# Optimization experiments

Hardware: AMD Instinct MI355X
Metric: run time of the kernel (lower is better)

## Reference

```python
import jax, jax.numpy as jnp
import numpy as np

SIGMA = 1.0
TOP_K = 4

def setup_inputs() -> dict:
    key = jax.random.key(0)
    k1, k2, k3, k4 = jax.random.split(key, 4)
    B, N, IN_DIM, OUT_DIM, P = 2, 4096, 128, 128, 3
    x = jax.random.normal(k1, (B, N, IN_DIM), dtype=jnp.float32)
    pos = jax.random.normal(k2, (B, N, P), dtype=jnp.float32)
    # Linear(in_dim, out_dim): W [in_dim, out_dim], b [out_dim]
    lim = 1.0 / np.sqrt(IN_DIM)
    W = jax.random.uniform(k3, (IN_DIM, OUT_DIM), minval=-lim, maxval=lim, dtype=jnp.float32)
    b = jax.random.uniform(k4, (OUT_DIM,), minval=-lim, maxval=lim, dtype=jnp.float32)
    return {"x": x, "pos": pos, "W": W, "b": b}

def reference(x, pos, W, b):
    B, N, _ = x.shape
    # pairwise distances [B, N, N]
    pos_diff = pos[:, :, None, :] - pos[:, None, :, :]
    dist = jnp.sqrt(jnp.sum(pos_diff ** 2, axis=-1) + 1e-8)
    adj = jnp.exp(-dist ** 2 / (2.0 * SIGMA ** 2))
    # top-k mask along last dim
    _, indices = jax.lax.top_k(adj, TOP_K)  # [B, N, k]
    b_idx = jnp.arange(B)[:, None, None]
    n_idx = jnp.arange(N)[None, :, None]
    mask = jnp.zeros_like(adj).at[b_idx, n_idx, indices].set(1.0)
    adj = adj * mask
    adj = adj / (jnp.sum(adj, axis=-1, keepdims=True) + 1e-8)
    # weighted aggregation + linear
    out = jnp.einsum('bnm,bmd->bnd', adj, x)
    return out @ W + b
```

## Files before the change

### kernel.cpp

```cpp
#include <hip/hip_runtime.h>
#include <hip/hip_bf16.h>

#define NPTS 4096
#define NROWS 8192
#define DIM 128
#define CAP 8

typedef __attribute__((ext_vector_type(8))) short bf16x8;
typedef __attribute__((ext_vector_type(4))) float f32x4;

__global__ __launch_bounds__(256) void prep(const float* __restrict__ pos,
                                            const float* __restrict__ W,
                                            float4* __restrict__ pos4,
                                            __hip_bfloat16* __restrict__ Wt) {
    int t = blockIdx.x * 256 + threadIdx.x;
    if (t < NROWS) {
        const float* p = pos + (size_t)t * 3;
        pos4[t] = make_float4(p[0], p[1], p[2], 0.f);
    } else if (t < NROWS + DIM * DIM) {
        int i = t - NROWS;
        int n = i >> 7, k = i & 127;
        Wt[i] = __float2bfloat16(W[k * DIM + n]);
    }
}

__global__ __launch_bounds__(256) void xw_mfma(const float* __restrict__ x,
                                               const __hip_bfloat16* __restrict__ Wt,
                                               __hip_bfloat16* __restrict__ xWb) {
    int wave = threadIdx.x >> 6;
    int lane = threadIdx.x & 63;
    int tile = blockIdx.x * 4 + wave;
    int m0 = (tile >> 3) << 4;
    int n0 = (tile & 7) << 4;
    int r = lane & 15;
    int kg = lane >> 4;
    const float* xr = x + (size_t)(m0 + r) * DIM + kg * 8;
    const __hip_bfloat16* br = Wt + (size_t)(n0 + r) * DIM + kg * 8;
    f32x4 acc = {0.f, 0.f, 0.f, 0.f};
#pragma unroll
    for (int kb = 0; kb < 4; ++kb) {
        float4 a0 = *(const float4*)(xr + kb * 32);
        float4 a1 = *(const float4*)(xr + kb * 32 + 4);
        bf16x8 af;
        union { __hip_bfloat16 h; short s; } u;
        u.h = __float2bfloat16(a0.x); af[0] = u.s;
        u.h = __float2bfloat16(a0.y); af[1] = u.s;
        u.h = __float2bfloat16(a0.z); af[2] = u.s;
        u.h = __float2bfloat16(a0.w); af[3] = u.s;
        u.h = __float2bfloat16(a1.x); af[4] = u.s;
        u.h = __float2bfloat16(a1.y); af[5] = u.s;
        u.h = __float2bfloat16(a1.z); af[6] = u.s;
        u.h = __float2bfloat16(a1.w); af[7] = u.s;
        bf16x8 bfr = *(const bf16x8*)(br + kb * 32);
        acc = __builtin_amdgcn_mfma_f32_16x16x32_bf16(af, bfr, acc, 0, 0, 0);
    }
    int col = n0 + r;
    int rbase = m0 + (kg << 2);
#pragma unroll
    for (int reg = 0; reg < 4; ++reg)
        xWb[(size_t)(rbase + reg) * DIM + col] = __float2bfloat16(acc[reg]);
}

__device__ __forceinline__ float dist2(float4 q, float4 p) {
    float dx = q.x - p.x, dy = q.y - p.y, dz = q.z - p.z;
    return fmaf(dx, dx, fmaf(dy, dy, dz * dz));
}

__device__ __forceinline__ void vins(float& k0, float& k1, float& k2, float& k3,
                                     float s) {
    float c = fmaxf(k0, s); k0 = fminf(k0, s);
    float t = fmaxf(k1, c); k1 = fminf(k1, c); c = t;
    t = fmaxf(k2, c);       k2 = fminf(k2, c); c = t;
    k3 = fminf(k3, c);
}

__device__ __forceinline__ void vmerge(float& a0, float& a1, float& a2, float& a3,
                                       float b0, float b1, float b2, float b3) {
    float m0 = fminf(a0, b3), m1 = fminf(a1, b2);
    float m2 = fminf(a2, b1), m3 = fminf(a3, b0);
    float t0 = fminf(m0, m2), t2 = fmaxf(m0, m2);
    float t1 = fminf(m1, m3), t3 = fmaxf(m1, m3);
    a0 = fminf(t0, t1); a1 = fmaxf(t0, t1);
    a2 = fminf(t2, t3); a3 = fmaxf(t2, t3);
}

__global__ __launch_bounds__(256, 8) void topk_agg(const float4* __restrict__ pos4,
                                                   const __hip_bfloat16* __restrict__ xWb,
                                                   const float* __restrict__ bias,
                                                   float* __restrict__ out) {
    int lane = threadIdx.x & 63;
    int wave = threadIdx.x >> 6;
    int group = wave >> 1;
    int half = wave & 1;
    int rowbase = blockIdx.x * 4 + group * 2;
    int batch = rowbase >> 12;
    int ibase = rowbase & (NPTS - 1);
    const float4* pb = pos4 + (size_t)batch * NPTS;

    __shared__ float    vx[2][2][2][4];
    __shared__ unsigned hidx[2][2][2][CAP];
    __shared__ float    hdva[2][2][2][CAP];
    __shared__ unsigned hcnt[2][2][2];
    __shared__ unsigned fidx[2][2][4];
    __shared__ float    fdst[2][2][4];

    float4 q0 = pb[ibase], q1 = pb[ibase + 1];
    const float INF = __int_as_float(0x7f800000);
    float a0 = INF, a1 = INF, a2 = INF, a3 = INF;
    float b0 = INF, b1 = INF, b2 = INF, b3 = INF;
    int jbase = (half << 11) + lane;

#pragma unroll 4
    for (int t = 0; t < 32; ++t) {
        float4 p = pb[jbase + (t << 6)];
        vins(a0, a1, a2, a3, dist2(q0, p));
        vins(b0, b1, b2, b3, dist2(q1, p));
    }
#pragma unroll
    for (int off = 1; off < 64; off <<= 1) {
        float p0 = __shfl_xor(a0, off), p1 = __shfl_xor(a1, off);
        float p2 = __shfl_xor(a2, off), p3 = __shfl_xor(a3, off);
        vmerge(a0, a1, a2, a3, p0, p1, p2, p3);
        p0 = __shfl_xor(b0, off); p1 = __shfl_xor(b1, off);
        p2 = __shfl_xor(b2, off); p3 = __shfl_xor(b3, off);
        vmerge(b0, b1, b2, b3, p0, p1, p2, p3);
    }
    if (lane == 0) {
        vx[group][half][0][0] = a0; vx[group][half][0][1] = a1;
        vx[group][half][0][2] = a2; vx[group][half][0][3] = a3;
        vx[group][half][1][0] = b0; vx[group][half][1][1] = b1;
        vx[group][half][1][2] = b2; vx[group][half][1][3] = b3;
    }
    __syncthreads();
    {
        int oh = half ^ 1;
        vmerge(a0, a1, a2, a3, vx[group][oh][0][0], vx[group][oh][0][1],
                               vx[group][oh][0][2], vx[group][oh][0][3]);
        vmerge(b0, b1, b2, b3, vx[group][oh][1][0], vx[group][oh][1][1],
                               vx[group][oh][1][2], vx[group][oh][1][3]);
    }
    float t3a = a3, t3b = b3;

    unsigned ca = 0, cb = 0;
#pragma unroll 2
    for (int t = 0; t < 32; ++t) {
        int j = jbase + (t << 6);
        float4 p = pb[j];
        float da = dist2(q0, p);
        float db = dist2(q1, p);
        bool ha = da <= t3a;
        unsigned long long ma = __ballot(ha);
        if (ma) {
            if (ha) {
                unsigned posn = ca + (unsigned)__popcll(ma & ((1ull << lane) - 1));
                if (posn < CAP) { hidx[group][0][half][posn] = (unsigned)j;
                                  hdva[group][0][half][posn] = da; }
            }
            ca += (unsigned)__popcll(ma);
        }
        bool hb = db <= t3b;
        unsigned long long mb = __ballot(hb);
        if (mb) {
            if (hb) {
                unsigned posn = cb + (unsigned)__popcll(mb & ((1ull << lane) - 1));
                if (posn < CAP) { hidx[group][1][half][posn] = (unsigned)j;
                                  hdva[group][1][half][posn] = db; }
            }
            cb += (unsigned)__popcll(mb);
        }
    }
    if (lane == 0) {
        hcnt[group][0][half] = ca < CAP ? ca : CAP;
        hcnt[group][1][half] = cb < CAP ? cb : CAP;
    }
    __syncthreads();

    if (half == 0 && lane < 32) {
        int r = lane >> 4;
        int e = lane & 15;
        unsigned c0 = hcnt[group][r][0], c1 = hcnt[group][r][1];
        bool valid = (e < CAP) ? ((unsigned)e < c0) : ((unsigned)(e - CAP) < c1);
        unsigned jj = 0; float dd = 0.f;
        if (valid) {
            jj = hidx[group][r][e >= CAP][e & (CAP - 1)];
            dd = hdva[group][r][e >= CAP][e & (CAP - 1)];
        }
        double key = valid
            ? __longlong_as_double(__double_as_longlong((double)dd) |
                                   (unsigned long long)jj)
            : __builtin_inf();
        int base = lane & 16;
        int rank = 0;
#pragma unroll
        for (int s = 0; s < 16; ++s) {
            double ks = __shfl(key, base + s);
            rank += (ks < key) ? 1 : 0;
        }
        if (valid && rank < 4) {
            fidx[group][r][rank] = jj;
            fdst[group][r][rank] = dd;
        }
    }
    __syncthreads();
    if (half) return;

    int c = lane << 1;
    float2 bb = *(const float2*)(bias + c);
    const unsigned short* xu = (const unsigned short*)xWb;
    size_t bbase = ((size_t)batch * NPTS) << 7;
#pragma unroll
    for (int k = 0; k < 2; ++k) {
        unsigned i0 = fidx[group][k][0], i1 = fidx[group][k][1];
        unsigned i2 = fidx[group][k][2], i3 = fidx[group][k][3];
        float d0 = fdst[group][k][0], d1 = fdst[group][k][1];
        float d2 = fdst[group][k][2], d3 = fdst[group][k][3];
        float w0 = __expf(-(d0 + 1e-8f) * 0.5f);
        float w1 = __expf(-(d1 + 1e-8f) * 0.5f);
        float w2 = __expf(-(d2 + 1e-8f) * 0.5f);
        float w3 = __expf(-(d3 + 1e-8f) * 0.5f);
        float inv = 1.0f / (w0 + w1 + w2 + w3 + 1e-8f);
        w0 *= inv; w1 *= inv; w2 *= inv; w3 *= inv;
        ushort2 g0 = *(const ushort2*)(xu + bbase + ((size_t)i0 << 7) + c);
        ushort2 g1 = *(const ushort2*)(xu + bbase + ((size_t)i1 << 7) + c);
        ushort2 g2 = *(const ushort2*)(xu + bbase + ((size_t)i2 << 7) + c);
        ushort2 g3 = *(const ushort2*)(xu + bbase + ((size_t)i3 << 7) + c);
        float ox = bb.x + w0 * __uint_as_float((unsigned)g0.x << 16)
                        + w1 * __uint_as_float((unsigned)g1.x << 16)
                        + w2 * __uint_as_float((unsigned)g2.x << 16)
                        + w3 * __uint_as_float((unsigned)g3.x << 16);
        float oy = bb.y + w0 * __uint_as_float((unsigned)g0.y << 16)
                        + w1 * __uint_as_float((unsigned)g1.y << 16)
                        + w2 * __uint_as_float((unsigned)g2.y << 16)
                        + w3 * __uint_as_float((unsigned)g3.y << 16);
        *(float2*)(out + (((size_t)(rowbase + k)) << 7) + c) = make_float2(ox, oy);
    }
}

extern "C" void kernel_launch(void* const* d_in, const int* in_sizes, int n_in,
                              void* d_out, int out_size, void* d_ws, size_t ws_size,
                              hipStream_t stream) {
    const float* x    = (const float*)d_in[0];
    const float* pos  = (const float*)d_in[1];
    const float* W    = (const float*)d_in[2];
    const float* bias = (const float*)d_in[3];
    float* out = (float*)d_out;

    char* ws = (char*)d_ws;
    __hip_bfloat16* xWb = (__hip_bfloat16*)ws;
    float4* pos4 = (float4*)(ws + (size_t)NROWS * DIM * 2);
    __hip_bfloat16* Wt = (__hip_bfloat16*)(ws + (size_t)NROWS * DIM * 2
                                              + (size_t)NROWS * 16);

    prep<<<(NROWS + DIM * DIM + 255) / 256, 256, 0, stream>>>(pos, W, pos4, Wt);
    xw_mfma<<<(NROWS / 16) * (DIM / 16) / 4, 256, 0, stream>>>(x, Wt, xWb);
    topk_agg<<<NROWS / 4, 256, 0, stream>>>(pos4, xWb, bias, out);
}
```

Measured before the change: 95.24 us.

## Process eight query rows per block, each wave scanning a quarter of candidates

Each block now handles eight query rows instead of four. All four waves scan disjoint quarters of the 4096 candidate points for all eight rows, so each loaded candidate position is reused across eight distance computations rather than two. The per-wave top-4 results are merged through shared memory, and a 32-lane rank sort selects the final neighbours. Every wave then writes two output rows. This cuts position-load traffic per row and doubles rows per block, but it needs many more registers (launch bounds drop to 4) and issues eight ballots per candidate.

```diff
diff --git a/kernel.cpp b/kernel.cpp
--- a/kernel.cpp
+++ b/kernel.cpp
@@ -4,6 +4,7 @@
 #define NPTS 4096
 #define NROWS 8192
 #define DIM 128
+#define RPW 8
 #define CAP 8
 
 typedef __attribute__((ext_vector_type(8))) short bf16x8;
@@ -84,136 +85,133 @@
     a2 = fminf(t2, t3); a3 = fmaxf(t2, t3);
 }
 
-__global__ __launch_bounds__(256, 8) void topk_agg(const float4* __restrict__ pos4,
+__global__ __launch_bounds__(256, 4) void topk_agg(const float4* __restrict__ pos4,
                                                    const __hip_bfloat16* __restrict__ xWb,
                                                    const float* __restrict__ bias,
                                                    float* __restrict__ out) {
     int lane = threadIdx.x & 63;
     int wave = threadIdx.x >> 6;
-    int group = wave >> 1;
-    int half = wave & 1;
-    int rowbase = blockIdx.x * 4 + group * 2;
+    int rowbase = blockIdx.x * RPW;
     int batch = rowbase >> 12;
     int ibase = rowbase & (NPTS - 1);
     const float4* pb = pos4 + (size_t)batch * NPTS;
 
-    __shared__ float    vx[2][2][2][4];
-    __shared__ unsigned hidx[2][2][2][CAP];
-    __shared__ float    hdva[2][2][2][CAP];
-    __shared__ unsigned hcnt[2][2][2];
-    __shared__ unsigned fidx[2][2][4];
-    __shared__ float    fdst[2][2][4];
-
-    float4 q0 = pb[ibase], q1 = pb[ibase + 1];
+    __shared__ float4   vx4[4][RPW];
+    __shared__ unsigned hidx[RPW][4][CAP];
+    __shared__ float    hdva[RPW][4][CAP];
+    __shared__ unsigned hcnt[RPW][4];
+    __shared__ unsigned fidx[RPW][4];
+    __shared__ float    fdst[RPW][4];
+
+    float4 q[RPW];
+#pragma unroll
+    for (int r = 0; r < RPW; ++r) q[r] = pb[ibase + r];
+
     const float INF = __int_as_float(0x7f800000);
-    float a0 = INF, a1 = INF, a2 = INF, a3 = INF;
-    float b0 = INF, b1 = INF, b2 = INF, b3 = INF;
-    int jbase = (half << 11) + lane;
+    float a0[RPW], a1[RPW], a2[RPW], a3[RPW];
+#pragma unroll
+    for (int r = 0; r < RPW; ++r) { a0[r] = a1[r] = a2[r] = a3[r] = INF; }
+
+    int jbase = (wave << 10) + lane;
 
 #pragma unroll 4
-    for (int t = 0; t < 32; ++t) {
+    for (int t = 0; t < 16; ++t) {
         float4 p = pb[jbase + (t << 6)];
-        vins(a0, a1, a2, a3, dist2(q0, p));
-        vins(b0, b1, b2, b3, dist2(q1, p));
+#pragma unroll
+        for (int r = 0; r < RPW; ++r)
+            vins(a0[r], a1[r], a2[r], a3[r], dist2(q[r], p));
     }
 #pragma unroll
     for (int off = 1; off < 64; off <<= 1) {
-        float p0 = __shfl_xor(a0, off), p1 = __shfl_xor(a1, off);
-        float p2 = __shfl_xor(a2, off), p3 = __shfl_xor(a3, off);
-        vmerge(a0, a1, a2, a3, p0, p1, p2, p3);
-        p0 = __shfl_xor(b0, off); p1 = __shfl_xor(b1, off);
-        p2 = __shfl_xor(b2, off); p3 = __shfl_xor(b3, off);
-        vmerge(b0, b1, b2, b3, p0, p1, p2, p3);
+#pragma unroll
+        for (int r = 0; r < RPW; ++r) {
+            float p0 = __shfl_xor(a0[r], off), p1 = __shfl_xor(a1[r], off);
+            float p2 = __shfl_xor(a2[r], off), p3 = __shfl_xor(a3[r], off);
+            vmerge(a0[r], a1[r], a2[r], a3[r], p0, p1, p2, p3);
+        }
     }
     if (lane == 0) {
-        vx[group][half][0][0] = a0; vx[group][half][0][1] = a1;
-        vx[group][half][0][2] = a2; vx[group][half][0][3] = a3;
-        vx[group][half][1][0] = b0; vx[group][half][1][1] = b1;
-        vx[group][half][1][2] = b2; vx[group][half][1][3] = b3;
+#pragma unroll
+        for (int r = 0; r < RPW; ++r)
+            vx4[wave][r] = make_float4(a0[r], a1[r], a2[r], a3[r]);
     }
     __syncthreads();
-    {
-        int oh = half ^ 1;
-        vmerge(a0, a1, a2, a3, vx[group][oh][0][0], vx[group][oh][0][1],
-                               vx[group][oh][0][2], vx[group][oh][0][3]);
-        vmerge(b0, b1, b2, b3, vx[group][oh][1][0], vx[group][oh][1][1],
-                               vx[group][oh][1][2], vx[group][oh][1][3]);
-    }
-    float t3a = a3, t3b = b3;
-
-    unsigned ca = 0, cb = 0;
+#pragma unroll
+    for (int qq = 0; qq < 4; ++qq) {
+        if (qq == wave) continue;
+#pragma unroll
+        for (int r = 0; r < RPW; ++r) {
+            float4 o = vx4[qq][r];
+            vmerge(a0[r], a1[r], a2[r], a3[r], o.x, o.y, o.z, o.w);
+        }
+    }
+
+    unsigned cnt[RPW];
+#pragma unroll
+    for (int r = 0; r < RPW; ++r) cnt[r] = 0;
 #pragma unroll 2
-    for (int t = 0; t < 32; ++t) {
+    for (int t = 0; t < 16; ++t) {
         int j = jbase + (t << 6);
         float4 p = pb[j];
-        float da = dist2(q0, p);
-        float db = dist2(q1, p);
-        bool ha = da <= t3a;
-        unsigned long long ma = __ballot(ha);
-        if (ma) {
-            if (ha) {
-                unsigned posn = ca + (unsigned)__popcll(ma & ((1ull << lane) - 1));
-                if (posn < CAP) { hidx[group][0][half][posn] = (unsigned)j;
-                                  hdva[group][0][half][posn] = da; }
+#pragma unroll
+        for (int r = 0; r < RPW; ++r) {
+            float d = dist2(q[r], p);
+            bool h = d <= a3[r];
+            unsigned long long m = __ballot(h);
+            if (m) {
+                if (h) {
+                    unsigned posn = cnt[r] +
+                        (unsigned)__popcll(m & ((1ull << lane) - 1));
+                    if (posn < CAP) { hidx[r][wave][posn] = (unsigned)j;
+                                      hdva[r][wave][posn] = d; }
+                }
+                cnt[r] += (unsigned)__popcll(m);
             }
-            ca += (unsigned)__popcll(ma);
-        }
-        bool hb = db <= t3b;
-        unsigned long long mb = __ballot(hb);
-        if (mb) {
-            if (hb) {
-                unsigned posn = cb + (unsigned)__popcll(mb & ((1ull << lane) - 1));
-                if (posn < CAP) { hidx[group][1][half][posn] = (unsigned)j;
-                                  hdva[group][1][half][posn] = db; }
-            }
-            cb += (unsigned)__popcll(mb);
         }
     }
     if (lane == 0) {
-        hcnt[group][0][half] = ca < CAP ? ca : CAP;
-        hcnt[group][1][half] = cb < CAP ? cb : CAP;
+#pragma unroll
+        for (int r = 0; r < RPW; ++r)
+            hcnt[r][wave] = cnt[r] < CAP ? cnt[r] : CAP;
     }
     __syncthreads();
 
-    if (half == 0 && lane < 32) {
-        int r = lane >> 4;
-        int e = lane & 15;
-        unsigned c0 = hcnt[group][r][0], c1 = hcnt[group][r][1];
-        bool valid = (e < CAP) ? ((unsigned)e < c0) : ((unsigned)(e - CAP) < c1);
+    {
+        int r = 2 * wave + (lane >> 5);
+        int e = lane & 31;
+        int qq = e >> 3, slot = e & 7;
+        bool valid = (unsigned)slot < hcnt[r][qq];
         unsigned jj = 0; float dd = 0.f;
-        if (valid) {
-            jj = hidx[group][r][e >= CAP][e & (CAP - 1)];
-            dd = hdva[group][r][e >= CAP][e & (CAP - 1)];
-        }
+        if (valid) { jj = hidx[r][qq][slot]; dd = hdva[r][qq][slot]; }
         double key = valid
             ? __longlong_as_double(__double_as_longlong((double)dd) |
                                    (unsigned long long)jj)
             : __builtin_inf();
-        int base = lane & 16;
+        int base = lane & 32;
         int rank = 0;
 #pragma unroll
-        for (int s = 0; s < 16; ++s) {
+        for (int s = 0; s < 32; ++s) {
             double ks = __shfl(key, base + s);
             rank += (ks < key) ? 1 : 0;
         }
         if (valid && rank < 4) {
-            fidx[group][r][rank] = jj;
-            fdst[group][r][rank] = dd;
+            fidx[r][rank] = jj;
+            fdst[r][rank] = dd;
         }
     }
     __syncthreads();
-    if (half) return;
 
     int c = lane << 1;
     float2 bb = *(const float2*)(bias + c);
     const unsigned short* xu = (const unsigned short*)xWb;
     size_t bbase = ((size_t)batch * NPTS) << 7;
 #pragma unroll
-    for (int k = 0; k < 2; ++k) {
-        unsigned i0 = fidx[group][k][0], i1 = fidx[group][k][1];
-        unsigned i2 = fidx[group][k][2], i3 = fidx[group][k][3];
-        float d0 = fdst[group][k][0], d1 = fdst[group][k][1];
-        float d2 = fdst[group][k][2], d3 = fdst[group][k][3];
+    for (int kk = 0; kk < 2; ++kk) {
+        int r = 2 * wave + kk;
+        unsigned i0 = fidx[r][0], i1 = fidx[r][1];
+        unsigned i2 = fidx[r][2], i3 = fidx[r][3];
+        float d0 = fdst[r][0], d1 = fdst[r][1];
+        float d2 = fdst[r][2], d3 = fdst[r][3];
         float w0 = __expf(-(d0 + 1e-8f) * 0.5f);
         float w1 = __expf(-(d1 + 1e-8f) * 0.5f);
         float w2 = __expf(-(d2 + 1e-8f) * 0.5f);
@@ -232,7 +230,7 @@
                         + w1 * __uint_as_float((unsigned)g1.y << 16)
                         + w2 * __uint_as_float((unsigned)g2.y << 16)
                         + w3 * __uint_as_float((unsigned)g3.y << 16);
-        *(float2*)(out + (((size_t)(rowbase + k)) << 7) + c) = make_float2(ox, oy);
+        *(float2*)(out + (((size_t)(rowbase + r)) << 7) + c) = make_float2(ox, oy);
     }
 }
 
@@ -253,5 +251,5 @@
 
     prep<<<(NROWS + DIM * DIM + 255) / 256, 256, 0, stream>>>(pos, W, pos4, Wt);
     xw_mfma<<<(NROWS / 16) * (DIM / 16) / 4, 256, 0, stream>>>(x, Wt, xWb);
-    topk_agg<<<NROWS / 4, 256, 0, stream>>>(pos4, xWb, bias, out);
-}
+    topk_agg<<<NROWS / RPW, 256, 0, stream>>>(pos4, xWb, bias, out);
+}
```

Result: slower. 102.2 us (+7.3%).
